# Kernel optimization log

Hardware: AMD Instinct MI355X
Metric: run time of the kernel (lower is better)

The kernel has to match this reference:

```python
import jax, jax.numpy as jnp
import numpy as np

B, T, H, NH, HD = 2, 2048, 2048, 16, 128


def setup_inputs() -> dict:
    key = jax.random.key(0)
    k1, k2, k3 = jax.random.split(key, 3)
    hidden_states = jax.random.normal(k1, (B, T, H), dtype=jnp.float32)
    w_qkv = jax.random.normal(k2, (3 * H, H), dtype=jnp.float32) * (1.0 / np.sqrt(H))
    w_out = jax.random.normal(k3, (H, H), dtype=jnp.float32) * (1.0 / np.sqrt(H))
    return {"hidden_states": hidden_states, "w_qkv": w_qkv, "w_out": w_out}


def reference(hidden_states, w_qkv, w_out):
    scale = 1.0 / np.sqrt(HD)
    # qkv projection: torch Linear is x @ W.T with W [out, in]
    qkv = jnp.einsum('bth,oh->bto', hidden_states, w_qkv)  # [B, T, 3H]
    q, k, v = jnp.split(qkv, 3, axis=2)
    # [B, NH, T, HD]
    q = q.reshape(B, T, NH, HD).transpose(0, 2, 1, 3)
    k = k.reshape(B, T, NH, HD).transpose(0, 2, 1, 3)
    v = v.reshape(B, T, NH, HD).transpose(0, 2, 1, 3)
    scores = jnp.einsum('bhqd,bhkd->bhqk', q, k) * scale  # [B, NH, T, T]
    mask = jnp.tril(jnp.ones((T, T), dtype=bool))  # causal
    scores = jnp.where(mask[None, None], scores, -jnp.inf)
    probs = jax.nn.softmax(scores, axis=-1)
    attn = jnp.einsum('bhqk,bhkd->bhqd', probs, v)  # [B, NH, T, HD]
    attn = attn.transpose(0, 2, 1, 3).reshape(B, T, H)
    out = jnp.einsum('bth,oh->bto', attn, w_out)
    return out
```

## Files before the change

### kernel.cpp

```cpp
#include <hip/hip_runtime.h>
#include <cstdint>
#include <cstddef>

typedef _Float16 f16x8 __attribute__((ext_vector_type(8)));
typedef _Float16 f16x4 __attribute__((ext_vector_type(4)));
typedef float    f32x4 __attribute__((ext_vector_type(4)));
typedef unsigned short ushort_t;

#define LOG2E 1.4426950408889634f

constexpr int BATCH = 2;
constexpr int TSEQ  = 2048;
constexpr int HID   = 2048;
constexpr int NH    = 16;
constexpr int HD    = 128;
constexpr int GK    = 2048;
constexpr int NKT   = GK / 64;

__device__ inline f32x4 mfma16(f16x8 a, f16x8 b, f32x4 c) {
    return __builtin_amdgcn_mfma_f32_16x16x32_f16(a, b, c, 0, 0, 0);
}

__device__ inline void async_copy16(const void* src, void* dst_lds) {
    __builtin_amdgcn_global_load_lds(
        (const __attribute__((address_space(1))) uint32_t*)src,
        (__attribute__((address_space(3))) uint32_t*)dst_lds, 16, 0, 0);
}

__global__ __launch_bounds__(256)
void cast_all(const float4* __restrict__ hs, const float4* __restrict__ wqkv,
              const float4* __restrict__ wout, f16x4* __restrict__ hs_h,
              f16x4* __restrict__ wqkv_h, f16x4* __restrict__ wout_h,
              int n_hs, int n_wqkv, int n_wout) {
    int i = blockIdx.x * 256 + threadIdx.x;
    const float4* src; f16x4* dst; int j;
    if (i < n_hs)                 { src = hs;   dst = hs_h;   j = i; }
    else if (i < n_hs + n_wqkv)   { src = wqkv; dst = wqkv_h; j = i - n_hs; }
    else if (i < n_hs + n_wqkv + n_wout) { src = wout; dst = wout_h; j = i - n_hs - n_wqkv; }
    else return;
    float4 v = src[j];
    f16x4 o = { (_Float16)v.x, (_Float16)v.y, (_Float16)v.z, (_Float16)v.w };
    dst[j] = o;
}

template <int MODE>
__global__ __launch_bounds__(256, 2)
void gemm_bt(const _Float16* __restrict__ A, const _Float16* __restrict__ B,
             float* __restrict__ C, _Float16* __restrict__ Qo,
             _Float16* __restrict__ Ko, _Float16* __restrict__ Vo, int NB) {
    __shared__ __align__(16) _Float16 As[2][128 * 64];
    __shared__ __align__(16) _Float16 Bs[2][128 * 64];

    const int tid  = threadIdx.x;
    const int lane = tid & 63;
    const int w    = tid >> 6;
    const int l15  = lane & 15;
    const int lq   = lane >> 4;
    const int wr   = w >> 1, wc = w & 1;

    const int bid = (int)blockIdx.x;
    const int cpx = (int)gridDim.x >> 3;
    const int swz = (bid & 7) * cpx + (bid >> 3);
    const int bn  = swz % NB, bm = swz / NB;
    const int m0  = bm * 128, n0 = bn * 128;

    const _Float16* Ab = A + (size_t)m0 * GK;
    const _Float16* Bb = B + (size_t)n0 * GK;

    auto stage = [&](int t, int b) {
        const int k0 = t * 64;
        #pragma unroll
        for (int it = 0; it < 4; ++it) {
            const int slot = it * 256 + tid;
            const int row = slot >> 3, c16 = slot & 7;
            const int srcb = c16 ^ (row & 7);
            async_copy16(Ab + (size_t)row * GK + k0 + srcb * 8,
                         (char*)As[b] + slot * 16);
        }
        #pragma unroll
        for (int it = 0; it < 4; ++it) {
            const int slot = it * 256 + tid;
            const int row = slot >> 3, c16 = slot & 7;
            const int srcb = c16 ^ (row & 7);
            async_copy16(Bb + (size_t)row * GK + k0 + srcb * 8,
                         (char*)Bs[b] + slot * 16);
        }
    };

    f32x4 acc[4][4] = {};

    stage(0, 0);
    stage(1, 1);

    for (int t = 0; t < NKT; ++t) {
        const int cur = t & 1;
        if (t + 1 < NKT) asm volatile("s_waitcnt vmcnt(8)" ::: "memory");
        else             asm volatile("s_waitcnt vmcnt(0)" ::: "memory");
        __builtin_amdgcn_s_barrier();
        __builtin_amdgcn_sched_barrier(0);

        const char* At_ = (const char*)As[cur];
        const char* Bt_ = (const char*)Bs[cur];

        f16x8 af[4][2], bff[4][2];
        #pragma unroll
        for (int i = 0; i < 4; ++i)
            #pragma unroll
            for (int kk = 0; kk < 2; ++kk) {
                const int ra = wr * 64 + i * 16 + l15;
                af[i][kk]  = *(const f16x8*)(At_ + ra * 128 + (((kk * 4 + lq) ^ (ra & 7)) << 4));
                const int rb = wc * 64 + i * 16 + l15;
                bff[i][kk] = *(const f16x8*)(Bt_ + rb * 128 + (((kk * 4 + lq) ^ (rb & 7)) << 4));
            }
        asm volatile("s_waitcnt lgkmcnt(0)" ::: "memory");
        __builtin_amdgcn_sched_barrier(0);
        __builtin_amdgcn_s_barrier();
        __builtin_amdgcn_sched_barrier(0);

        if (t + 2 < NKT) stage(t + 2, cur);

        __builtin_amdgcn_s_setprio(1);
        #pragma unroll
        for (int kk = 0; kk < 2; ++kk)
            #pragma unroll
            for (int i = 0; i < 4; ++i)
                #pragma unroll
                for (int j = 0; j < 4; ++j)
                    acc[i][j] = mfma16(af[i][kk], bff[j][kk], acc[i][j]);
        __builtin_amdgcn_s_setprio(0);
    }

    if (MODE == 0) {
        #pragma unroll
        for (int j = 0; j < 4; ++j) {
            const int ncol = n0 + wc * 64 + j * 16 + l15;
            const int which = ncol >> 11;
            const int oo = ncol & 2047;
            const int head = oo >> 7;
            const int d = oo & 127;
            _Float16* dst = (which == 0) ? Qo : (which == 1) ? Ko : Vo;
            const float scl = (which == 0) ? 0.08838834764831845f : 1.0f;
            #pragma unroll
            for (int i = 0; i < 4; ++i) {
                #pragma unroll
                for (int r = 0; r < 4; ++r) {
                    const int m = m0 + wr * 64 + i * 16 + lq * 4 + r;
                    const int b = m >> 11, tt = m & 2047;
                    dst[((size_t)(b * NH + head) * TSEQ + tt) * HD + d] =
                        (_Float16)(acc[i][j][r] * scl);
                }
            }
        }
    } else {
        #pragma unroll
        for (int i = 0; i < 4; ++i)
            #pragma unroll
            for (int j = 0; j < 4; ++j)
                #pragma unroll
                for (int r = 0; r < 4; ++r) {
                    const int m = m0 + wr * 64 + i * 16 + lq * 4 + r;
                    const int n = n0 + wc * 64 + j * 16 + l15;
                    C[(size_t)m * HID + n] = acc[i][j][r];
                }
    }
}

__global__ __launch_bounds__(256)
void attn_fwd(const _Float16* __restrict__ Q, const _Float16* __restrict__ K,
              const _Float16* __restrict__ V, _Float16* __restrict__ O) {
    __shared__ __align__(16) char Ks[64 * 256];
    __shared__ __align__(16) char Vt[128 * 128];
    __shared__ __align__(16) char Ps[4][2048];

    const int tid  = threadIdx.x;
    const int lane = tid & 63;
    const int w    = tid >> 6;
    const int l15  = lane & 15;
    const int lq   = lane >> 4;

    const int bh   = (int)blockIdx.x & 31;
    const int pair = (int)blockIdx.x >> 5;
    const int b = bh >> 4, h = bh & 15;

    const size_t base = (size_t)bh * TSEQ * HD;
    const _Float16* Qp = Q + base;
    const _Float16* Kp = K + base;
    const _Float16* Vp = V + base;

    const f16x8 ones = { (_Float16)1.f, (_Float16)1.f, (_Float16)1.f, (_Float16)1.f,
                         (_Float16)1.f, (_Float16)1.f, (_Float16)1.f, (_Float16)1.f };

    uint4 vv[4];
    auto loadV = [&](int t) {
        const int row = tid & 63;
        #pragma unroll
        for (int it = 0; it < 4; ++it) {
            const int c8 = w * 4 + it;
            vv[it] = *(const uint4*)(Vp + (size_t)(t * 64 + row) * HD + c8 * 8);
        }
    };
    auto stageK = [&](int t) {
        #pragma unroll
        for (int it = 0; it < 4; ++it) {
            const int slot = it * 256 + tid;
            const int row = slot >> 4, c16 = slot & 15;
            const int srcb = c16 ^ (row & 7);
            async_copy16(Kp + (size_t)(t * 64 + row) * HD + srcb * 8, Ks + slot * 16);
        }
    };
    auto writeV = [&]() {
        const int row = tid & 63;
        #pragma unroll
        for (int it = 0; it < 4; ++it) {
            const int c8 = w * 4 + it;
            const uint32_t wrd[4] = {vv[it].x, vv[it].y, vv[it].z, vv[it].w};
            #pragma unroll
            for (int p2 = 0; p2 < 4; ++p2) {
                const int d0 = c8 * 8 + p2 * 2, d1 = d0 + 1;
                int b0 = d0 * 128 + row * 2; b0 ^= (d0 & 7) << 4;
                int b1 = d1 * 128 + row * 2; b1 ^= (d1 & 7) << 4;
                *(ushort_t*)(Vt + b0) = (ushort_t)(wrd[p2] & 0xffffu);
                *(ushort_t*)(Vt + b1) = (ushort_t)(wrd[p2] >> 16);
            }
        }
    };

    char* Pb = Ps[w];

    for (int phase = 0; phase < 2; ++phase) {
        const int qt = phase ? pair : (31 - pair);
        const int q0 = qt * 64;
        const int NT = qt + 1;

        if (phase) __syncthreads();

        const int qrow = q0 + w * 16 + l15;
        f16x8 qf[4];
        #pragma unroll
        for (int ks = 0; ks < 4; ++ks)
            qf[ks] = *(const f16x8*)(Qp + (size_t)qrow * HD + ks * 32 + lq * 8);

        f32x4 o[8] = {};
        f32x4 osum = {};
        float m_run[4];
        #pragma unroll
        for (int r = 0; r < 4; ++r) m_run[r] = -1e30f;

        stageK(0);
        loadV(0);

        for (int t = 0; t < NT; ++t) {
            writeV();
            __syncthreads();
            if (t + 1 < NT) loadV(t + 1);

            const int kv0 = t * 64;
            f32x4 s[4] = {};
            __builtin_amdgcn_s_setprio(1);
            #pragma unroll
            for (int ks = 0; ks < 4; ++ks) {
                #pragma unroll
                for (int nf = 0; nf < 4; ++nf) {
                    const int r   = nf * 16 + l15;
                    const int blk = (ks * 4 + lq) ^ (r & 7);
                    const f16x8 kf = *(const f16x8*)(Ks + r * 256 + blk * 16);
                    s[nf] = mfma16(qf[ks], kf, s[nf]);
                }
            }
            __builtin_amdgcn_s_setprio(0);

            if (kv0 + 63 > q0 + w * 16) {
                #pragma unroll
                for (int nf = 0; nf < 4; ++nf) {
                    const int kvp = kv0 + nf * 16 + l15;
                    #pragma unroll
                    for (int r = 0; r < 4; ++r)
                        if (kvp > q0 + w * 16 + lq * 4 + r) s[nf][r] = -1e30f;
                }
            }

            bool need = false;
            #pragma unroll
            for (int r = 0; r < 4; ++r) {
                const float v = fmaxf(fmaxf(s[0][r], s[1][r]), fmaxf(s[2][r], s[3][r]));
                need = need || (v > m_run[r] + 5.0f);
            }
            if (__any(need)) {
                float alpha[4];
                #pragma unroll
                for (int r = 0; r < 4; ++r) {
                    float v = fmaxf(fmaxf(s[0][r], s[1][r]), fmaxf(s[2][r], s[3][r]));
                    v = fmaxf(v, __shfl_xor(v, 1));
                    v = fmaxf(v, __shfl_xor(v, 2));
                    v = fmaxf(v, __shfl_xor(v, 4));
                    v = fmaxf(v, __shfl_xor(v, 8));
                    const float mn = fmaxf(m_run[r], v);
                    alpha[r] = __builtin_exp2f((m_run[r] - mn) * LOG2E);
                    m_run[r] = mn;
                }
                #pragma unroll
                for (int df = 0; df < 8; ++df)
                    #pragma unroll
                    for (int r = 0; r < 4; ++r)
                        o[df][r] *= alpha[r];
                #pragma unroll
                for (int r = 0; r < 4; ++r) osum[r] *= alpha[r];
            }

            #pragma unroll
            for (int nf = 0; nf < 4; ++nf) {
                #pragma unroll
                for (int r = 0; r < 4; ++r) {
                    const float p = __builtin_exp2f((s[nf][r] - m_run[r]) * LOG2E);
                    const int qp = lq * 4 + r;
                    int byt = qp * 128 + (nf * 16 + l15) * 2;
                    byt ^= (qp & 7) << 4;
                    union { _Float16 hf; ushort_t u; } cv;
                    cv.hf = (_Float16)p;
                    *(ushort_t*)(Pb + byt) = cv.u;
                }
            }

            __builtin_amdgcn_s_setprio(1);
            #pragma unroll
            for (int ks2 = 0; ks2 < 2; ++ks2) {
                const int pblk = (ks2 * 4 + lq) ^ (l15 & 7);
                const f16x8 pf = *(const f16x8*)(Pb + l15 * 128 + pblk * 16);
                #pragma unroll
                for (int df = 0; df < 8; ++df) {
                    const int vr   = df * 16 + l15;
                    const int vblk = (ks2 * 4 + lq) ^ (vr & 7);
                    const f16x8 vf = *(const f16x8*)(Vt + vr * 128 + vblk * 16);
                    o[df] = mfma16(pf, vf, o[df]);
                }
                osum = mfma16(pf, ones, osum);
            }
            __builtin_amdgcn_s_setprio(0);

            if (t + 1 < NT) {
                __syncthreads();
                stageK(t + 1);
            }
        }

        float rl[4];
        #pragma unroll
        for (int r = 0; r < 4; ++r) rl[r] = 1.0f / osum[r];
        #pragma unroll
        for (int df = 0; df < 8; ++df) {
            #pragma unroll
            for (int r = 0; r < 4; ++r) {
                const int qg = q0 + w * 16 + lq * 4 + r;
                const int dg = df * 16 + l15;
                O[((size_t)(b * TSEQ + qg)) * HID + h * HD + dg] =
                    (_Float16)(o[df][r] * rl[r]);
            }
        }
    }
}

extern "C" void kernel_launch(void* const* d_in, const int* in_sizes, int n_in,
                              void* d_out, int out_size, void* d_ws, size_t ws_size,
                              hipStream_t stream) {
    (void)in_sizes; (void)n_in; (void)out_size; (void)ws_size;
    const float* hs   = (const float*)d_in[0];
    const float* wqkv = (const float*)d_in[1];
    const float* wout = (const float*)d_in[2];

    char* ws = (char*)d_ws;
    size_t off = 0;
    _Float16* hs_h   = (_Float16*)(ws + off); off += (size_t)BATCH * TSEQ * HID * 2;
    _Float16* wqkv_h = (_Float16*)(ws + off); off += (size_t)3 * HID * HID * 2;
    _Float16* wout_h = (_Float16*)(ws + off); off += (size_t)HID * HID * 2;
    _Float16* Qh     = (_Float16*)(ws + off); off += (size_t)BATCH * NH * TSEQ * HD * 2;
    _Float16* Kh     = (_Float16*)(ws + off); off += (size_t)BATCH * NH * TSEQ * HD * 2;
    _Float16* Vh     = (_Float16*)(ws + off); off += (size_t)BATCH * NH * TSEQ * HD * 2;
    _Float16* At     = (_Float16*)(ws + off); off += (size_t)BATCH * TSEQ * HID * 2;

    const int n4_hs   = BATCH * TSEQ * HID / 4;
    const int n4_wqkv = 3 * HID * HID / 4;
    const int n4_wout = HID * HID / 4;
    const int n4_all  = n4_hs + n4_wqkv + n4_wout;
    cast_all<<<dim3((n4_all + 255) / 256), dim3(256), 0, stream>>>(
        (const float4*)hs, (const float4*)wqkv, (const float4*)wout,
        (f16x4*)hs_h, (f16x4*)wqkv_h, (f16x4*)wout_h, n4_hs, n4_wqkv, n4_wout);

    gemm_bt<0><<<dim3(1536), dim3(256), 0, stream>>>(
        hs_h, wqkv_h, nullptr, Qh, Kh, Vh, 48);

    attn_fwd<<<dim3(512), dim3(256), 0, stream>>>(Qh, Kh, Vh, At);

    gemm_bt<1><<<dim3(512), dim3(256), 0, stream>>>(
        At, wout_h, (float*)d_out, nullptr, nullptr, nullptr, 16);
}
```

Measured before the change: 265.8 us.

## Use 256x128 triple-buffered tile with 512 threads for QKV projection GEMM

The QKV projection GEMM now uses 512-thread blocks computing 256x128 output tiles, so each loaded B (weight) tile is reused across twice as many rows. LDS staging goes from double to triple buffering, which lets the loop drop the second per-iteration barrier and the lgkmcnt wait before issuing the next prefetch. The output projection keeps the old 128x128 kernel as a separate, simplified gemm_small. The larger LDS footprint (about 144KB per block) limits the kernel to one block per CU and raises register pressure.

```diff
diff --git a/kernel.cpp b/kernel.cpp
--- a/kernel.cpp
+++ b/kernel.cpp
@@ -44,12 +44,12 @@
 }
 
 template <int MODE>
-__global__ __launch_bounds__(256, 2)
-void gemm_bt(const _Float16* __restrict__ A, const _Float16* __restrict__ B,
-             float* __restrict__ C, _Float16* __restrict__ Qo,
-             _Float16* __restrict__ Ko, _Float16* __restrict__ Vo, int NB) {
-    __shared__ __align__(16) _Float16 As[2][128 * 64];
-    __shared__ __align__(16) _Float16 Bs[2][128 * 64];
+__global__ __launch_bounds__(512, 2)
+void gemm_big(const _Float16* __restrict__ A, const _Float16* __restrict__ B,
+              float* __restrict__ C, _Float16* __restrict__ Qo,
+              _Float16* __restrict__ Ko, _Float16* __restrict__ Vo, int NB) {
+    __shared__ __align__(16) _Float16 As[3][256 * 64];
+    __shared__ __align__(16) _Float16 Bs[3][128 * 64];
 
     const int tid  = threadIdx.x;
     const int lane = tid & 63;
@@ -62,7 +62,7 @@
     const int cpx = (int)gridDim.x >> 3;
     const int swz = (bid & 7) * cpx + (bid >> 3);
     const int bn  = swz % NB, bm = swz / NB;
-    const int m0  = bm * 128, n0 = bn * 128;
+    const int m0  = bm * 256, n0 = bn * 128;
 
     const _Float16* Ab = A + (size_t)m0 * GK;
     const _Float16* Bb = B + (size_t)n0 * GK;
@@ -71,15 +71,15 @@
         const int k0 = t * 64;
         #pragma unroll
         for (int it = 0; it < 4; ++it) {
-            const int slot = it * 256 + tid;
+            const int slot = it * 512 + tid;
             const int row = slot >> 3, c16 = slot & 7;
             const int srcb = c16 ^ (row & 7);
             async_copy16(Ab + (size_t)row * GK + k0 + srcb * 8,
                          (char*)As[b] + slot * 16);
         }
         #pragma unroll
-        for (int it = 0; it < 4; ++it) {
-            const int slot = it * 256 + tid;
+        for (int it = 0; it < 2; ++it) {
+            const int slot = it * 512 + tid;
             const int row = slot >> 3, c16 = slot & 7;
             const int srcb = c16 ^ (row & 7);
             async_copy16(Bb + (size_t)row * GK + k0 + srcb * 8,
@@ -93,14 +93,13 @@
     stage(1, 1);
 
     for (int t = 0; t < NKT; ++t) {
-        const int cur = t & 1;
-        if (t + 1 < NKT) asm volatile("s_waitcnt vmcnt(8)" ::: "memory");
+        if (t + 1 < NKT) asm volatile("s_waitcnt vmcnt(6)" ::: "memory");
         else             asm volatile("s_waitcnt vmcnt(0)" ::: "memory");
         __builtin_amdgcn_s_barrier();
         __builtin_amdgcn_sched_barrier(0);
 
-        const char* At_ = (const char*)As[cur];
-        const char* Bt_ = (const char*)Bs[cur];
+        const char* At_ = (const char*)As[t % 3];
+        const char* Bt_ = (const char*)Bs[t % 3];
 
         f16x8 af[4][2], bff[4][2];
         #pragma unroll
@@ -112,12 +111,8 @@
                 const int rb = wc * 64 + i * 16 + l15;
                 bff[i][kk] = *(const f16x8*)(Bt_ + rb * 128 + (((kk * 4 + lq) ^ (rb & 7)) << 4));
             }
-        asm volatile("s_waitcnt lgkmcnt(0)" ::: "memory");
-        __builtin_amdgcn_sched_barrier(0);
-        __builtin_amdgcn_s_barrier();
-        __builtin_amdgcn_sched_barrier(0);
-
-        if (t + 2 < NKT) stage(t + 2, cur);
+
+        if (t + 2 < NKT) stage(t + 2, (t + 2) % 3);
 
         __builtin_amdgcn_s_setprio(1);
         #pragma unroll
@@ -163,6 +158,104 @@
                     C[(size_t)m * HID + n] = acc[i][j][r];
                 }
     }
+}
+
+template <int MODE>
+__global__ __launch_bounds__(256, 2)
+void gemm_small(const _Float16* __restrict__ A, const _Float16* __restrict__ B,
+                float* __restrict__ C, int NB) {
+    __shared__ __align__(16) _Float16 As[2][128 * 64];
+    __shared__ __align__(16) _Float16 Bs[2][128 * 64];
+
+    const int tid  = threadIdx.x;
+    const int lane = tid & 63;
+    const int w    = tid >> 6;
+    const int l15  = lane & 15;
+    const int lq   = lane >> 4;
+    const int wr   = w >> 1, wc = w & 1;
+
+    const int bid = (int)blockIdx.x;
+    const int cpx = (int)gridDim.x >> 3;
+    const int swz = (bid & 7) * cpx + (bid >> 3);
+    const int bn  = swz % NB, bm = swz / NB;
+    const int m0  = bm * 128, n0 = bn * 128;
+
+    const _Float16* Ab = A + (size_t)m0 * GK;
+    const _Float16* Bb = B + (size_t)n0 * GK;
+
+    auto stage = [&](int t, int b) {
+        const int k0 = t * 64;
+        #pragma unroll
+        for (int it = 0; it < 4; ++it) {
+            const int slot = it * 256 + tid;
+            const int row = slot >> 3, c16 = slot & 7;
+            const int srcb = c16 ^ (row & 7);
+            async_copy16(Ab + (size_t)row * GK + k0 + srcb * 8,
+                         (char*)As[b] + slot * 16);
+        }
+        #pragma unroll
+        for (int it = 0; it < 4; ++it) {
+            const int slot = it * 256 + tid;
+            const int row = slot >> 3, c16 = slot & 7;
+            const int srcb = c16 ^ (row & 7);
+            async_copy16(Bb + (size_t)row * GK + k0 + srcb * 8,
+                         (char*)Bs[b] + slot * 16);
+        }
+    };
+
+    f32x4 acc[4][4] = {};
+
+    stage(0, 0);
+    stage(1, 1);
+
+    for (int t = 0; t < NKT; ++t) {
+        const int cur = t & 1;
+        if (t + 1 < NKT) asm volatile("s_waitcnt vmcnt(8)" ::: "memory");
+        else             asm volatile("s_waitcnt vmcnt(0)" ::: "memory");
+        __builtin_amdgcn_s_barrier();
+        __builtin_amdgcn_sched_barrier(0);
+
+        const char* At_ = (const char*)As[cur];
+        const char* Bt_ = (const char*)Bs[cur];
+
+        f16x8 af[4][2], bff[4][2];
+        #pragma unroll
+        for (int i = 0; i < 4; ++i)
+            #pragma unroll
+            for (int kk = 0; kk < 2; ++kk) {
+                const int ra = wr * 64 + i * 16 + l15;
+                af[i][kk]  = *(const f16x8*)(At_ + ra * 128 + (((kk * 4 + lq) ^ (ra & 7)) << 4));
+                const int rb = wc * 64 + i * 16 + l15;
+                bff[i][kk] = *(const f16x8*)(Bt_ + rb * 128 + (((kk * 4 + lq) ^ (rb & 7)) << 4));
+            }
+        asm volatile("s_waitcnt lgkmcnt(0)" ::: "memory");
+        __builtin_amdgcn_sched_barrier(0);
+        __builtin_amdgcn_s_barrier();
+        __builtin_amdgcn_sched_barrier(0);
+
+        if (t + 2 < NKT) stage(t + 2, cur);
+
+        __builtin_amdgcn_s_setprio(1);
+        #pragma unroll
+        for (int kk = 0; kk < 2; ++kk)
+            #pragma unroll
+            for (int i = 0; i < 4; ++i)
+                #pragma unroll
+                for (int j = 0; j < 4; ++j)
+                    acc[i][j] = mfma16(af[i][kk], bff[j][kk], acc[i][j]);
+        __builtin_amdgcn_s_setprio(0);
+    }
+
+    #pragma unroll
+    for (int i = 0; i < 4; ++i)
+        #pragma unroll
+        for (int j = 0; j < 4; ++j)
+            #pragma unroll
+            for (int r = 0; r < 4; ++r) {
+                const int m = m0 + wr * 64 + i * 16 + lq * 4 + r;
+                const int n = n0 + wc * 64 + j * 16 + l15;
+                C[(size_t)m * HID + n] = acc[i][j][r];
+            }
 }
 
 __global__ __launch_bounds__(256)
@@ -385,11 +478,11 @@
         (const float4*)hs, (const float4*)wqkv, (const float4*)wout,
         (f16x4*)hs_h, (f16x4*)wqkv_h, (f16x4*)wout_h, n4_hs, n4_wqkv, n4_wout);
 
-    gemm_bt<0><<<dim3(1536), dim3(256), 0, stream>>>(
+    gemm_big<0><<<dim3(768), dim3(512), 0, stream>>>(
         hs_h, wqkv_h, nullptr, Qh, Kh, Vh, 48);
 
     attn_fwd<<<dim3(512), dim3(256), 0, stream>>>(Qh, Kh, Vh, At);
 
-    gemm_bt<1><<<dim3(512), dim3(256), 0, stream>>>(
-        At, wout_h, (float*)d_out, nullptr, nullptr, nullptr, 16);
-}
+    gemm_small<1><<<dim3(512), dim3(256), 0, stream>>>(
+        At, wout_h, (float*)d_out, 16);
+}
```

After: 262.9 us. No clear change (-1.1%).
